# Performance work log

Measured on AMD Instinct MI355X. Metric: run time of the kernel, lower is better.

The kernel has to match this reference:

```python
import jax, jax.numpy as jnp
import numpy as np

P, B, A, NT = 2, 96, 32, 24
N = B * A
MD, MA, MW = 4, 4, 2
NPOLB = MD + MA
C_LK = 0.089793561062583294  # 1 / (2 * pi**1.5)


def _norm(v):
    return v / jnp.sqrt(jnp.sum(v * v, -1, keepdims=True) + 1e-12)


def _gat_atoms(c, i):
    # c: [P,B,A,3], i: [P,B,K] -> [P,B,K,3]
    return jnp.take_along_axis(c, jnp.broadcast_to(i[..., None], i.shape + (3,)), axis=2)


def setup_inputs():
    key = jax.random.key(0)
    rng = np.random.default_rng(0)
    inp = {}
    inp["pose_coords"] = jax.random.normal(key, (P, N, 3), jnp.float32) * 8.0
    inp["pose_stack_block_type"] = jnp.asarray(rng.integers(0, NT, (P, B)), jnp.int32)
    inp["pose_stack_min_bond_separation"] = jnp.full((P, B, B), 6, jnp.int32)
    inp["bt_n_atoms"] = jnp.full((NT,), A, jnp.int32)
    bonds = np.stack([np.arange(A), (np.arange(A) + 1) % A], -1)
    inp["bt_all_bonds"] = jnp.asarray(np.broadcast_to(bonds, (NT, A, 2)).copy(), jnp.int32)
    rngs = np.stack([np.arange(A), np.arange(A) + 1], -1)
    inp["bt_atom_all_bond_ranges"] = jnp.asarray(np.broadcast_to(rngs, (NT, A, 2)).copy(), jnp.int32)
    inp["bt_tile_n_donH"] = jnp.asarray(rng.integers(1, MD + 1, (NT,)), jnp.int32)
    inp["bt_tile_n_acc"] = jnp.asarray(rng.integers(1, MA + 1, (NT,)), jnp.int32)
    donH = np.broadcast_to(2 * np.arange(MD) + 1, (NT, MD)).copy()
    inp["bt_tile_donH_inds"] = jnp.asarray(donH, jnp.int32)
    inp["bt_tile_don_hvy_inds"] = jnp.asarray(donH - 1, jnp.int32)
    inp["bt_tile_acc_inds"] = jnp.asarray(np.broadcast_to(8 + np.arange(MA), (NT, MA)).copy(), jnp.int32)
    inp["bt_tile_hybridization"] = jnp.asarray(rng.integers(0, 3, (NT, MA)), jnp.int32)
    is_h = np.zeros((NT, A), np.int32)
    is_h[:, 1:8:2] = 1
    inp["bt_atom_is_hydrogen"] = jnp.asarray(is_h)
    par = np.empty((NT, A, 4), np.float32)
    par[..., 0] = rng.uniform(1.4, 2.2, (NT, A))   # lj_radius
    par[..., 1] = rng.uniform(-6.0, 6.0, (NT, A))  # lk_dgfree
    par[..., 2] = rng.uniform(3.0, 3.6, (NT, A))   # lk_lambda
    par[..., 3] = rng.uniform(3.0, 15.0, (NT, A))  # lk_volume
    inp["bt_tile_lk_ball_params"] = jnp.asarray(par)
    pd = np.minimum(np.abs(np.arange(A)[:, None] - np.arange(A)[None, :]), 6)
    inp["bt_path_distance"] = jnp.asarray(np.broadcast_to(pd, (NT, A, A)).copy(), jnp.int32)
    inp["lk_ball_global_params"] = jnp.asarray([6.0, 3.709, 2.828], jnp.float32)   # cutoff, ramp_width_A2, d2_low
    inp["water_gen_global_params"] = jnp.asarray([2.65, 2.0943951], jnp.float32)   # water dist, water bond angle
    inp["sp2_water_tors"] = jnp.asarray([0.0, np.pi], jnp.float32)
    inp["sp3_water_tors"] = jnp.asarray([np.pi / 3.0, -np.pi / 3.0], jnp.float32)
    inp["ring_water_tors"] = jnp.asarray([0.0, np.pi / 2.0], jnp.float32)
    return inp


def reference(pose_coords, pose_stack_block_type, pose_stack_min_bond_separation,
              bt_n_atoms, bt_all_bonds, bt_atom_all_bond_ranges,
              bt_tile_n_donH, bt_tile_n_acc, bt_tile_donH_inds, bt_tile_don_hvy_inds,
              bt_tile_acc_inds, bt_tile_hybridization, bt_atom_is_hydrogen,
              bt_tile_lk_ball_params, bt_path_distance,
              lk_ball_global_params, water_gen_global_params,
              sp2_water_tors, sp3_water_tors, ring_water_tors):
    bt = pose_stack_block_type
    coords = pose_coords.reshape(P, B, A, 3)
    wdist = water_gen_global_params[0]
    wang = water_gen_global_params[1]
    # ---- step 1a: donor waters placed along heavy->H direction ----
    hvy_i = bt_tile_don_hvy_inds[bt]
    H_i = bt_tile_donH_inds[bt]                                              # [P,B,MD]
    hvy = _gat_atoms(coords, hvy_i)
    Hxyz = _gat_atoms(coords, H_i)
    don_w = hvy + wdist * _norm(Hxyz - hvy)                                  # [P,B,MD,3]
    don_mask = jnp.arange(MD) < bt_tile_n_donH[bt][..., None]                # [P,B,MD]
    don_w = jnp.broadcast_to(don_w[..., None, :], (P, B, MD, MW, 3))
    don_wm = don_mask[..., None] & (jnp.arange(MW) == 0)                     # one water per donH
    # ---- step 1b: acceptor waters via hybridization-dependent torsion (NeRF) ----
    acc_i = bt_tile_acc_inds[bt]                                             # [P,B,MA]
    ranges0 = bt_atom_all_bond_ranges[bt][..., 0]                            # [P,B,A]
    bonds1 = bt_all_bonds[bt][..., 1]                                        # [P,B,A]
    base_i = jnp.take_along_axis(bonds1, jnp.take_along_axis(ranges0, acc_i, axis=2), axis=2)
    base2_i = jnp.take_along_axis(bonds1, jnp.take_along_axis(ranges0, base_i, axis=2), axis=2)
    cxyz = _gat_atoms(coords, acc_i)
    bxyz = _gat_atoms(coords, base_i)
    axyz = _gat_atoms(coords, base2_i)
    e1 = _norm(cxyz - bxyz)
    nrm = _norm(jnp.cross(bxyz - axyz, e1))
    e2 = jnp.cross(nrm, e1)
    tors_tab = jnp.stack([sp2_water_tors, sp3_water_tors, ring_water_tors])  # [3,MW]
    chi = tors_tab[bt_tile_hybridization[bt]]                                # [P,B,MA,MW]
    ct, st = jnp.cos(wang), jnp.sin(wang)
    acc_w = (cxyz[..., None, :]
             + (-wdist * ct) * e1[..., None, :]
             + (wdist * st) * jnp.cos(chi)[..., None] * e2[..., None, :]
             + (wdist * st) * jnp.sin(chi)[..., None] * nrm[..., None, :])   # [P,B,MA,MW,3]
    acc_mask = jnp.arange(MA) < bt_tile_n_acc[bt][..., None]
    acc_wm = jnp.broadcast_to(acc_mask[..., None], (P, B, MA, MW))
    # ---- assemble polar sites + waters ----
    waters = jnp.concatenate([don_w, acc_w], axis=2).reshape(P, B * NPOLB, MW, 3)
    wmask = jnp.concatenate([don_wm, acc_wm], axis=2).reshape(P, B * NPOLB, MW)
    pol_loc = jnp.concatenate([hvy_i, acc_i], axis=2)                        # [P,B,NPOLB]
    pol_mask = jnp.concatenate([don_mask, acc_mask], axis=2).reshape(P, B * NPOLB)
    gidx = (jnp.arange(B)[None, :, None] * A + pol_loc).reshape(P, B * NPOLB)
    # ---- gather per-atom data ----
    params_flat = bt_tile_lk_ball_params[bt].reshape(P, N, 4)
    heavy = bt_atom_is_hydrogen[bt].reshape(P, N) == 0
    xp = jnp.take_along_axis(pose_coords, jnp.broadcast_to(gidx[..., None], gidx.shape + (3,)), axis=1)
    pp = jnp.take_along_axis(params_flat, jnp.broadcast_to(gidx[..., None], gidx.shape + (4,)), axis=1)
    # ---- step 2: pair distances + bond-separation mask ----
    diff = xp[:, :, None, :] - pose_coords[:, None, :, :]                    # [P,NPOL,N,3]
    d2 = jnp.maximum(jnp.sum(diff * diff, -1), 1e-2)
    d = jnp.sqrt(d2)
    b_i = gidx // A
    a_i = gidx % A
    b_j = jnp.arange(N) // A
    a_j = jnp.arange(N) % A
    bti = jnp.take_along_axis(bt, b_i, axis=1)
    intra = bt_path_distance[bti[:, :, None], a_i[:, :, None], a_j[None, None, :]]
    inter = pose_stack_min_bond_separation[jnp.arange(P)[:, None, None], b_i[:, :, None], b_j[None, None, :]]
    sep = jnp.where(b_i[:, :, None] == b_j[None, None, :], intra, inter)
    cutoff = lk_ball_global_params[0]
    ramp2 = lk_ball_global_params[1]
    d2_low = lk_ball_global_params[2]
    mask = (sep >= 4) & heavy[:, None, :] & pol_mask[:, :, None] & (d < cutoff)
    # ---- isotropic LK desolvation of polar atom i by occluder j ----
    ri, dgi, lami = pp[..., 0], pp[..., 1], pp[..., 2]
    rj, volj = params_flat[..., 0], params_flat[..., 3]
    x = (d - (ri[:, :, None] + rj[:, None, :])) / lami[:, :, None]
    lk_iso = C_LK * dgi[:, :, None] * volj[:, None, :] / lami[:, :, None] * jnp.exp(-x * x) / d2
    lk_iso = jnp.where(mask, lk_iso, 0.0)
    # ---- lk-ball fraction from water-site occlusion ----
    wdiff = waters[:, :, :, None, :] - pose_coords[:, None, None, :, :]      # [P,NPOL,MW,N,3]
    d2w = jnp.sum(wdiff * wdiff, -1)
    d2w = jnp.where(wmask[..., None], d2w, 1e9)
    d2wmin = jnp.min(d2w, axis=2)                                            # [P,NPOL,N]
    wt = jnp.clip((d2_low + ramp2 - d2wmin) / ramp2, 0.0, 1.0)
    frac = wt * wt * (3.0 - 2.0 * wt)
    return jnp.stack([jnp.sum(lk_iso, (1, 2)), jnp.sum(lk_iso * frac, (1, 2))])  # [2,P]
```

## Files before the change

### kernel.cpp

```cpp
#include <hip/hip_runtime.h>
#include <math.h>

constexpr int P  = 2;
constexpr int B  = 96;
constexpr int A  = 32;
constexpr int N  = B * A;
constexpr int MD = 4;
constexpr int MA = 4;
constexpr int NPOL = MD + MA;
constexpr int SJ = 2;
constexpr int JS = N / SJ;
constexpr int JPT = JS / 256;
constexpr float C_LK = 0.0897935610625833f;

__global__ void zero_out_kernel(float* out) {
    int t = threadIdx.x;
    if (t < 2 * P) out[t] = 0.0f;
}

__global__ __launch_bounds__(256) void lkball_kernel(
    const float* __restrict__ pose_coords,
    const int*   __restrict__ block_type,
    const int*   __restrict__ min_sep,
    const int*   __restrict__ all_bonds,
    const int*   __restrict__ bond_ranges,
    const int*   __restrict__ n_donH,
    const int*   __restrict__ n_acc,
    const int*   __restrict__ donH_inds,
    const int*   __restrict__ don_hvy_inds,
    const int*   __restrict__ acc_inds,
    const int*   __restrict__ hyb,
    const int*   __restrict__ is_h,
    const float* __restrict__ lk_params,
    const int*   __restrict__ path_dist,
    const float* __restrict__ glob,
    const float* __restrict__ wglob,
    const float* __restrict__ sp2t,
    const float* __restrict__ sp3t,
    const float* __restrict__ ringt,
    float*       __restrict__ out)
{
    __shared__ float spolar[NPOL][16];
    __shared__ int   spolai[NPOL];
    __shared__ int   s_bt[B];
    __shared__ int   smsep[B];
    __shared__ int   spath[NPOL * A];
    __shared__ float red0[4], red1[4];

    const int bid   = blockIdx.x;
    const int p     = bid / (B * SJ);
    const int rem   = bid % (B * SJ);
    const int b     = rem / SJ;
    const int slice = rem % SJ;
    const int tid   = threadIdx.x;

    if (tid < NPOL) {
        const int k  = tid;
        const int bt = block_type[p * B + b];
        const float wdist = wglob[0];
        const float wang  = wglob[1];
        float xp[3], w0[3], w1[3];
        int   a_i, valid;
        if (k < MD) {
            valid = (k < n_donH[bt]) ? 1 : 0;
            const int hvy = don_hvy_inds[bt * MD + k];
            const int Hi  = donH_inds[bt * MD + k];
            a_i = hvy;
            const float* hc = pose_coords + (size_t)(p * N + b * A + hvy) * 3;
            const float* Hc = pose_coords + (size_t)(p * N + b * A + Hi) * 3;
            float dx = Hc[0] - hc[0], dy = Hc[1] - hc[1], dz = Hc[2] - hc[2];
            float inv = 1.0f / sqrtf(dx * dx + dy * dy + dz * dz + 1e-12f);
            xp[0] = hc[0]; xp[1] = hc[1]; xp[2] = hc[2];
            w0[0] = hc[0] + wdist * dx * inv;
            w0[1] = hc[1] + wdist * dy * inv;
            w0[2] = hc[2] + wdist * dz * inv;
            w1[0] = hc[0] + 1.0e3f; w1[1] = hc[1] + 1.0e3f; w1[2] = hc[2] + 1.0e3f;
        } else {
            const int kk = k - MD;
            valid = (kk < n_acc[bt]) ? 1 : 0;
            const int ai = acc_inds[bt * MA + kk];
            a_i = ai;
            const int r0    = bond_ranges[(bt * A + ai) * 2 + 0];
            const int base  = all_bonds[(bt * A + r0) * 2 + 1];
            const int r0b   = bond_ranges[(bt * A + base) * 2 + 0];
            const int base2 = all_bonds[(bt * A + r0b) * 2 + 1];
            const float* c  = pose_coords + (size_t)(p * N + b * A + ai)    * 3;
            const float* bx = pose_coords + (size_t)(p * N + b * A + base)  * 3;
            const float* ax = pose_coords + (size_t)(p * N + b * A + base2) * 3;

            float e1x = c[0] - bx[0], e1y = c[1] - bx[1], e1z = c[2] - bx[2];
            float inv1 = 1.0f / sqrtf(e1x * e1x + e1y * e1y + e1z * e1z + 1e-12f);
            e1x *= inv1; e1y *= inv1; e1z *= inv1;

            float ux = bx[0] - ax[0], uy = bx[1] - ax[1], uz = bx[2] - ax[2];
            float nx = uy * e1z - uz * e1y;
            float ny = uz * e1x - ux * e1z;
            float nz = ux * e1y - uy * e1x;
            float inv2 = 1.0f / sqrtf(nx * nx + ny * ny + nz * nz + 1e-12f);
            nx *= inv2; ny *= inv2; nz *= inv2;
            float e2x = ny * e1z - nz * e1y;
            float e2y = nz * e1x - nx * e1z;
            float e2z = nx * e1y - ny * e1x;

            const int hy = hyb[bt * MA + kk];
            const float* tab = (hy == 0) ? sp2t : ((hy == 1) ? sp3t : ringt);
            const float ct = cosf(wang), st = sinf(wang);
            float c0 = cosf(tab[0]), s0 = sinf(tab[0]);
            float c1 = cosf(tab[1]), s1 = sinf(tab[1]);

            xp[0] = c[0]; xp[1] = c[1]; xp[2] = c[2];
            w0[0] = c[0] - wdist * ct * e1x + wdist * st * c0 * e2x + wdist * st * s0 * nx;
            w0[1] = c[1] - wdist * ct * e1y + wdist * st * c0 * e2y + wdist * st * s0 * ny;
            w0[2] = c[2] - wdist * ct * e1z + wdist * st * c0 * e2z + wdist * st * s0 * nz;
            w1[0] = c[0] - wdist * ct * e1x + wdist * st * c1 * e2x + wdist * st * s1 * nx;
            w1[1] = c[1] - wdist * ct * e1y + wdist * st * c1 * e2y + wdist * st * s1 * ny;
            w1[2] = c[2] - wdist * ct * e1z + wdist * st * c1 * e2z + wdist * st * s1 * nz;
        }
        const float* pr = lk_params + (size_t)(bt * A + a_i) * 4;
        const float lam = pr[2];
        spolar[k][0] = xp[0]; spolar[k][1] = xp[1]; spolar[k][2] = xp[2];
        spolar[k][3] = w0[0]; spolar[k][4] = w0[1]; spolar[k][5] = w0[2];
        spolar[k][6] = w1[0]; spolar[k][7] = w1[1]; spolar[k][8] = w1[2];
        spolar[k][9]  = pr[0];
        spolar[k][10] = valid ? (C_LK * pr[1] / lam) : 0.0f;
        spolar[k][11] = 1.0f / lam;
        spolai[k] = a_i;
    }
    if (tid >= 64 && tid < 64 + B)   s_bt[tid - 64]   = block_type[p * B + (tid - 64)];
    if (tid >= 160 && tid < 160 + B) smsep[tid - 160] = min_sep[(p * B + b) * B + (tid - 160)];
    __syncthreads();

    {
        const int k  = tid >> 5;
        const int aj = tid & 31;
        const int bt = s_bt[b];
        spath[tid] = path_dist[(bt * A + spolai[k]) * A + aj];
    }
    __syncthreads();

    const float cutoff = glob[0];
    const float inv_ramp2 = 1.0f / glob[1];
    const float c3 = glob[2] + glob[1];
    const int a_j = tid & 31;
    const int jbase = slice * JS + tid;

    float cx[JPT], cy[JPT], cz[JPT], rj[JPT], ve[JPT];
    float msep_f[JPT];
    int   intra[JPT];
#pragma unroll
    for (int i = 0; i < JPT; ++i) {
        const int j   = jbase + 256 * i;
        const int b_j = j >> 5;
        const float* cj = pose_coords + (size_t)(p * N + j) * 3;
        cx[i] = cj[0]; cy[i] = cj[1]; cz[i] = cj[2];
        const int bt_j = s_bt[b_j];
        const int hv   = is_h[bt_j * A + a_j];
        const float4 pj = *(const float4*)(lk_params + (size_t)(bt_j * A + a_j) * 4);
        rj[i] = pj.x;
        ve[i] = hv ? 0.0f : pj.w;
        msep_f[i] = (float)smsep[b_j];
        intra[i]  = (b_j == b);
    }

    float acc0 = 0.0f, acc1 = 0.0f;

#pragma unroll
    for (int k = 0; k < NPOL; ++k) {
        const float px = spolar[k][0], py = spolar[k][1], pz = spolar[k][2];
        const float w0x = spolar[k][3], w0y = spolar[k][4], w0z = spolar[k][5];
        const float w1x = spolar[k][6], w1y = spolar[k][7], w1z = spolar[k][8];
        const float ri = spolar[k][9], pref = spolar[k][10], inv_lam = spolar[k][11];
        const float path_k = (float)spath[k * A + a_j];

#pragma unroll
        for (int i = 0; i < JPT; ++i) {
            const float dx = px - cx[i], dy = py - cy[i], dz = pz - cz[i];
            float d2 = fmaf(dx, dx, fmaf(dy, dy, dz * dz));
            d2 = fmaxf(d2, 0.01f);
            const float d = __builtin_amdgcn_sqrtf(d2);
            const float sep = intra[i] ? path_k : msep_f[i];
            const bool ok = (sep >= 4.0f) & (d < cutoff);

            const float x = (d - ri - rj[i]) * inv_lam;
            float lk = pref * ve[i] * __expf(-x * x) * __builtin_amdgcn_rcpf(d2);
            lk = ok ? lk : 0.0f;

            const float d0x = w0x - cx[i], d0y = w0y - cy[i], d0z = w0z - cz[i];
            const float d1x = w1x - cx[i], d1y = w1y - cy[i], d1z = w1z - cz[i];
            const float d2w0 = fmaf(d0x, d0x, fmaf(d0y, d0y, d0z * d0z));
            const float d2w1 = fmaf(d1x, d1x, fmaf(d1y, d1y, d1z * d1z));
            const float d2wmin = fminf(d2w0, d2w1);
            float wt = (c3 - d2wmin) * inv_ramp2;
            wt = fminf(fmaxf(wt, 0.0f), 1.0f);
            const float frac = wt * wt * (3.0f - 2.0f * wt);

            acc0 += lk;
            acc1 = fmaf(lk, frac, acc1);
        }
    }

    for (int off = 32; off > 0; off >>= 1) {
        acc0 += __shfl_down(acc0, off);
        acc1 += __shfl_down(acc1, off);
    }
    const int wave = tid >> 6;
    const int lane = tid & 63;
    if (lane == 0) { red0[wave] = acc0; red1[wave] = acc1; }
    __syncthreads();
    if (tid == 0) {
        atomicAdd(&out[p],     red0[0] + red0[1] + red0[2] + red0[3]);
        atomicAdd(&out[P + p], red1[0] + red1[1] + red1[2] + red1[3]);
    }
}

extern "C" void kernel_launch(void* const* d_in, const int* in_sizes, int n_in,
                              void* d_out, int out_size, void* d_ws, size_t ws_size,
                              hipStream_t stream) {
    const float* pose_coords  = (const float*)d_in[0];
    const int*   block_type   = (const int*)  d_in[1];
    const int*   min_sep      = (const int*)  d_in[2];
    const int*   all_bonds    = (const int*)  d_in[4];
    const int*   bond_ranges  = (const int*)  d_in[5];
    const int*   n_donH       = (const int*)  d_in[6];
    const int*   n_acc        = (const int*)  d_in[7];
    const int*   donH_inds    = (const int*)  d_in[8];
    const int*   don_hvy_inds = (const int*)  d_in[9];
    const int*   acc_inds     = (const int*)  d_in[10];
    const int*   hyb          = (const int*)  d_in[11];
    const int*   is_h         = (const int*)  d_in[12];
    const float* lk_params    = (const float*)d_in[13];
    const int*   path_dist    = (const int*)  d_in[14];
    const float* glob         = (const float*)d_in[15];
    const float* wglob        = (const float*)d_in[16];
    const float* sp2t         = (const float*)d_in[17];
    const float* sp3t         = (const float*)d_in[18];
    const float* ringt        = (const float*)d_in[19];
    float* out = (float*)d_out;

    zero_out_kernel<<<1, 64, 0, stream>>>(out);

    const int nblocks = P * B * SJ;
    lkball_kernel<<<nblocks, 256, 0, stream>>>(
        pose_coords, block_type, min_sep, all_bonds, bond_ranges,
        n_donH, n_acc, donH_inds, don_hvy_inds, acc_inds, hyb, is_h,
        lk_params, path_dist, glob, wglob, sp2t, sp3t, ringt, out);
}
```

Measured before the change: 113.1 us.

## Specialize donor loop to one water, use rsq/exp2, deterministic two-pass reduction

Splits the polar loop so donor atoms (which have a single water site) skip the second water-distance computation. It replaces sqrt and rcp with a single rsq, folds the Gaussian exponent into exp2 with a precomputed negative scale, and compares squared distance against a squared cutoff. It also replaces the zero kernel plus global atomics with per-block partials in the workspace and a small reduce kernel. The donor split assumes the second water of donors is always masked, and the extra launch may add overhead.

```diff
diff --git a/kernel.cpp b/kernel.cpp
--- a/kernel.cpp
+++ b/kernel.cpp
@@ -11,12 +11,10 @@
 constexpr int SJ = 2;
 constexpr int JS = N / SJ;
 constexpr int JPT = JS / 256;
-constexpr float C_LK = 0.0897935610625833f;
-
-__global__ void zero_out_kernel(float* out) {
-    int t = threadIdx.x;
-    if (t < 2 * P) out[t] = 0.0f;
-}
+constexpr int NB = P * B * SJ;
+constexpr float C_LK  = 0.0897935610625833f;
+constexpr float LOG2E = 1.4426950408889634f;
+
 
 __global__ __launch_bounds__(256) void lkball_kernel(
     const float* __restrict__ pose_coords,
@@ -38,7 +36,7 @@
     const float* __restrict__ sp2t,
     const float* __restrict__ sp3t,
     const float* __restrict__ ringt,
-    float*       __restrict__ out)
+    float*       __restrict__ ws)
 {
     __shared__ float spolar[NPOL][16];
     __shared__ int   spolai[NPOL];
@@ -123,7 +121,7 @@
         spolar[k][6] = w1[0]; spolar[k][7] = w1[1]; spolar[k][8] = w1[2];
         spolar[k][9]  = pr[0];
         spolar[k][10] = valid ? (C_LK * pr[1] / lam) : 0.0f;
-        spolar[k][11] = 1.0f / lam;
+        spolar[k][11] = -LOG2E / (lam * lam);
         spolai[k] = a_i;
     }
     if (tid >= 64 && tid < 64 + B)   s_bt[tid - 64]   = block_type[p * B + (tid - 64)];
@@ -138,14 +136,13 @@
     }
     __syncthreads();
 
-    const float cutoff = glob[0];
+    const float cutoff2   = glob[0] * glob[0];
     const float inv_ramp2 = 1.0f / glob[1];
-    const float c3 = glob[2] + glob[1];
-    const int a_j = tid & 31;
+    const float c4        = (glob[2] + glob[1]) * inv_ramp2;
+    const int a_j   = tid & 31;
     const int jbase = slice * JS + tid;
 
-    float cx[JPT], cy[JPT], cz[JPT], rj[JPT], ve[JPT];
-    float msep_f[JPT];
+    float cx[JPT], cy[JPT], cz[JPT], rj[JPT], ve[JPT], msep_f[JPT];
     int   intra[JPT];
 #pragma unroll
     for (int i = 0; i < JPT; ++i) {
@@ -165,11 +162,13 @@
     float acc0 = 0.0f, acc1 = 0.0f;
 
 #pragma unroll
-    for (int k = 0; k < NPOL; ++k) {
-        const float px = spolar[k][0], py = spolar[k][1], pz = spolar[k][2];
-        const float w0x = spolar[k][3], w0y = spolar[k][4], w0z = spolar[k][5];
-        const float w1x = spolar[k][6], w1y = spolar[k][7], w1z = spolar[k][8];
-        const float ri = spolar[k][9], pref = spolar[k][10], inv_lam = spolar[k][11];
+    for (int k = 0; k < MD; ++k) {
+        const float4 q0 = ((const float4*)spolar[k])[0];
+        const float4 q1 = ((const float4*)spolar[k])[1];
+        const float4 q2 = ((const float4*)spolar[k])[2];
+        const float px  = q0.x, py  = q0.y, pz  = q0.z;
+        const float w0x = q0.w, w0y = q1.x, w0z = q1.y;
+        const float ri  = q2.y, pref = q2.z, negq = q2.w;
         const float path_k = (float)spath[k * A + a_j];
 
 #pragma unroll
@@ -177,12 +176,51 @@
             const float dx = px - cx[i], dy = py - cy[i], dz = pz - cz[i];
             float d2 = fmaf(dx, dx, fmaf(dy, dy, dz * dz));
             d2 = fmaxf(d2, 0.01f);
-            const float d = __builtin_amdgcn_sqrtf(d2);
+            const float rinv = __builtin_amdgcn_rsqf(d2);
+            const float d = d2 * rinv;
             const float sep = intra[i] ? path_k : msep_f[i];
-            const bool ok = (sep >= 4.0f) & (d < cutoff);
-
-            const float x = (d - ri - rj[i]) * inv_lam;
-            float lk = pref * ve[i] * __expf(-x * x) * __builtin_amdgcn_rcpf(d2);
+            const bool ok = (sep >= 4.0f) & (d2 < cutoff2);
+
+            const float t = d - ri - rj[i];
+            const float e = __builtin_amdgcn_exp2f(t * t * negq);
+            float lk = pref * ve[i] * e * (rinv * rinv);
+            lk = ok ? lk : 0.0f;
+
+            const float d0x = w0x - cx[i], d0y = w0y - cy[i], d0z = w0z - cz[i];
+            const float d2wmin = fmaf(d0x, d0x, fmaf(d0y, d0y, d0z * d0z));
+            float wt = fmaf(d2wmin, -inv_ramp2, c4);
+            wt = fminf(fmaxf(wt, 0.0f), 1.0f);
+            const float frac = wt * wt * fmaf(-2.0f, wt, 3.0f);
+
+            acc0 += lk;
+            acc1 = fmaf(lk, frac, acc1);
+        }
+    }
+
+#pragma unroll
+    for (int k = MD; k < NPOL; ++k) {
+        const float4 q0 = ((const float4*)spolar[k])[0];
+        const float4 q1 = ((const float4*)spolar[k])[1];
+        const float4 q2 = ((const float4*)spolar[k])[2];
+        const float px  = q0.x, py  = q0.y, pz  = q0.z;
+        const float w0x = q0.w, w0y = q1.x, w0z = q1.y;
+        const float w1x = q1.z, w1y = q1.w, w1z = q2.x;
+        const float ri  = q2.y, pref = q2.z, negq = q2.w;
+        const float path_k = (float)spath[k * A + a_j];
+
+#pragma unroll
+        for (int i = 0; i < JPT; ++i) {
+            const float dx = px - cx[i], dy = py - cy[i], dz = pz - cz[i];
+            float d2 = fmaf(dx, dx, fmaf(dy, dy, dz * dz));
+            d2 = fmaxf(d2, 0.01f);
+            const float rinv = __builtin_amdgcn_rsqf(d2);
+            const float d = d2 * rinv;
+            const float sep = intra[i] ? path_k : msep_f[i];
+            const bool ok = (sep >= 4.0f) & (d2 < cutoff2);
+
+            const float t = d - ri - rj[i];
+            const float e = __builtin_amdgcn_exp2f(t * t * negq);
+            float lk = pref * ve[i] * e * (rinv * rinv);
             lk = ok ? lk : 0.0f;
 
             const float d0x = w0x - cx[i], d0y = w0y - cy[i], d0z = w0z - cz[i];
@@ -190,9 +228,9 @@
             const float d2w0 = fmaf(d0x, d0x, fmaf(d0y, d0y, d0z * d0z));
             const float d2w1 = fmaf(d1x, d1x, fmaf(d1y, d1y, d1z * d1z));
             const float d2wmin = fminf(d2w0, d2w1);
-            float wt = (c3 - d2wmin) * inv_ramp2;
+            float wt = fmaf(d2wmin, -inv_ramp2, c4);
             wt = fminf(fmaxf(wt, 0.0f), 1.0f);
-            const float frac = wt * wt * (3.0f - 2.0f * wt);
+            const float frac = wt * wt * fmaf(-2.0f, wt, 3.0f);
 
             acc0 += lk;
             acc1 = fmaf(lk, frac, acc1);
@@ -208,9 +246,21 @@
     if (lane == 0) { red0[wave] = acc0; red1[wave] = acc1; }
     __syncthreads();
     if (tid == 0) {
-        atomicAdd(&out[p],     red0[0] + red0[1] + red0[2] + red0[3]);
-        atomicAdd(&out[P + p], red1[0] + red1[1] + red1[2] + red1[3]);
-    }
+        ws[bid]       = red0[0] + red0[1] + red0[2] + red0[3];
+        ws[512 + bid] = red1[0] + red1[1] + red1[2] + red1[3];
+    }
+}
+
+__global__ __launch_bounds__(256) void reduce_kernel(
+    const float* __restrict__ ws, float* __restrict__ out)
+{
+    const int wave = threadIdx.x >> 6;
+    const int lane = threadIdx.x & 63;
+    const int base = (wave & 1) * (B * SJ) + (wave >> 1) * 512;
+    float s = 0.0f;
+    for (int i = lane; i < B * SJ; i += 64) s += ws[base + i];
+    for (int off = 32; off > 0; off >>= 1) s += __shfl_down(s, off);
+    if (lane == 0) out[(wave >> 1) * P + (wave & 1)] = s;
 }
 
 extern "C" void kernel_launch(void* const* d_in, const int* in_sizes, int n_in,
@@ -236,12 +286,12 @@
     const float* sp3t         = (const float*)d_in[18];
     const float* ringt        = (const float*)d_in[19];
     float* out = (float*)d_out;
-
-    zero_out_kernel<<<1, 64, 0, stream>>>(out);
-
-    const int nblocks = P * B * SJ;
-    lkball_kernel<<<nblocks, 256, 0, stream>>>(
+    float* ws  = (float*)d_ws;
+
+    lkball_kernel<<<NB, 256, 0, stream>>>(
         pose_coords, block_type, min_sep, all_bonds, bond_ranges,
         n_donH, n_acc, donH_inds, don_hvy_inds, acc_inds, hyb, is_h,
-        lk_params, path_dist, glob, wglob, sp2t, sp3t, ringt, out);
+        lk_params, path_dist, glob, wglob, sp2t, sp3t, ringt, ws);
+
+    reduce_kernel<<<1, 256, 0, stream>>>(ws, out);
 }
```

New measurement: 106.7 us. 1.06x faster.
